# Performance work log

Measured on AMD Instinct MI355X. Metric: run time of the kernel, lower is better.

## Reference

```python
import jax, jax.numpy as jnp
import numpy as np

T, B, D, H = 4096, 4, 1024, 16


def setup_inputs() -> dict:
    key = jax.random.key(0)
    k0, k1, k2 = jax.random.split(key, 3)
    x = jax.random.normal(k0, (T, B, D), jnp.float32)
    Wqkv = jax.random.normal(k1, (3 * D, D), jnp.float32) * 0.02
    bqkv = jnp.zeros((3 * D,), jnp.float32)
    Wout = jax.random.normal(k2, (D, D), jnp.float32) * 0.02
    bout = jnp.zeros((D,), jnp.float32)
    return {"x": x, "Wqkv": Wqkv, "bqkv": bqkv, "Wout": Wout, "bout": bout, "nhead": H}


def reference(x, Wqkv, bqkv, Wout, bout, nhead):
    # x: (T, B, D) seq-first, query is key is value
    T_, B_, D_ = x.shape
    hd = D_ // nhead
    qkv = x @ Wqkv.T + bqkv                      # (T, B, 3D)
    q, k, v = jnp.split(qkv, 3, axis=-1)         # each (T, B, D)

    def heads(t):                                 # -> (B, H, T, hd)
        return t.reshape(T_, B_, nhead, hd).transpose(1, 2, 0, 3)

    q, k, v = heads(q), heads(k), heads(v)

    # Pearson correlation over the sequence axis: X, Y are (B, H, hd, T)
    X = jnp.swapaxes(q, -2, -1)
    Y = jnp.swapaxes(k, -2, -1)
    Xc = X - X.mean(-1, keepdims=True)
    Yc = Y - Y.mean(-1, keepdims=True)
    c = jnp.einsum('bhdt,bhet->bhde', Xc, Yc)    # (B, H, hd, hd)
    sx = (Xc ** 2).sum(-1)                       # (B, H, hd)
    sy = (Yc ** 2).sum(-1)                       # (B, H, hd)
    std = jnp.sqrt(sx[..., :, None] * sy[..., None, :])
    corr = jnp.clip(c / std, -1.0, 1.0)          # (B, H, hd, hd)

    attn = jnp.einsum('bhtd,bhde->bhte', v, corr)  # v @ corr: (B, H, T, hd)
    out = attn.transpose(2, 0, 1, 3).reshape(T_, B_, D_)  # (T, B, D)
    return out @ Wout.T + bout
```

## Files before the change

### kernel.cpp

```cpp
#include <hip/hip_runtime.h>
#include <hip/hip_bf16.h>

#define TDIM 4096
#define BDIM 4
#define DDIM 1024
#define HDIM 16
#define HD   64
#define MDIM (TDIM * BDIM)

typedef __attribute__((ext_vector_type(8))) short short8v;
typedef __attribute__((ext_vector_type(4))) float f32x4;

__device__ __forceinline__ ushort f2bfu(float f) {
  union { __hip_bfloat16 h; ushort u; } c;
  c.h = __float2bfloat16(f);
  return c.u;
}
__device__ __forceinline__ float bfu2f(ushort u) {
  union { ushort u; __hip_bfloat16 h; } c;
  c.u = u;
  return __bfloat162float(c.h);
}

#define GLOAD16(gp, lp) __builtin_amdgcn_global_load_lds( \
    (const __attribute__((address_space(1))) void*)(gp),  \
    (__attribute__((address_space(3))) void*)(lp), 16, 0, 0)

#define SWZ(row) (((row) >> 1) & 3)

__global__ __launch_bounds__(256)
void split_f32(const float* __restrict__ in, ushort* __restrict__ hi,
               ushort* __restrict__ lo, int n4)
{
  int i = blockIdx.x * blockDim.x + threadIdx.x;
  const int stride = gridDim.x * blockDim.x;
  for (; i < n4; i += stride) {
    const float4 v = ((const float4*)in)[i];
    ushort4 h, l;
    h.x = f2bfu(v.x); l.x = f2bfu(v.x - bfu2f(h.x));
    h.y = f2bfu(v.y); l.y = f2bfu(v.y - bfu2f(h.y));
    h.z = f2bfu(v.z); l.z = f2bfu(v.z - bfu2f(h.z));
    h.w = f2bfu(v.w); l.w = f2bfu(v.w - bfu2f(h.w));
    ((ushort4*)hi)[i] = h;
    ((ushort4*)lo)[i] = l;
  }
}

__global__ __launch_bounds__(256, 2)
void gemm1_mfma(const float* __restrict__ X, const ushort* __restrict__ Wh,
                const ushort* __restrict__ Wl, const float* __restrict__ bias,
                float* __restrict__ QK, ushort* __restrict__ Vh,
                ushort* __restrict__ Vl)
{
  __shared__ ushort sAh[128][32], sAl[128][32], sBh[128][32], sBl[128][32];
  const int tid = threadIdx.x;
  const int lane = tid & 63, wid = tid >> 6;
  const int m0 = blockIdx.y * 128, n0 = blockIdx.x * 128;
  const int ar = tid >> 3, aq = tid & 7;
  const int wm = wid >> 1, wn = wid & 1;
  const int fr = lane & 15, kg = lane >> 4;

  f32x4 acc[4][4];
#pragma unroll
  for (int m = 0; m < 4; ++m)
#pragma unroll
    for (int n = 0; n < 4; ++n) acc[m][n] = (f32x4){0.f, 0.f, 0.f, 0.f};

  for (int k0 = 0; k0 < DDIM; k0 += 32) {
    float4 av[4];
#pragma unroll
    for (int i = 0; i < 4; ++i)
      av[i] = *(const float4*)&X[(size_t)(m0 + ar + i * 32) * DDIM + k0 + aq * 4];
#pragma unroll
    for (int j = 0; j < 4; ++j) {
      const int c = wid * 4 + j;
      const int r0 = (c & 7) * 16;
      const int row = r0 + (lane >> 2);
      const int s = lane & 3;
      const size_t goff = (size_t)(n0 + row) * DDIM + k0 + ((s ^ SWZ(row)) << 3);
      if (c < 8) GLOAD16(Wh + goff, &sBh[r0][0]);
      else       GLOAD16(Wl + goff, &sBl[r0][0]);
    }
#pragma unroll
    for (int i = 0; i < 4; ++i) {
      const int row = ar + i * 32;
      const int sl = (((aq >> 1) ^ SWZ(row)) << 3) + ((aq & 1) << 2);
      ushort4 hv, lv;
      hv.x = f2bfu(av[i].x); lv.x = f2bfu(av[i].x - bfu2f(hv.x));
      hv.y = f2bfu(av[i].y); lv.y = f2bfu(av[i].y - bfu2f(hv.y));
      hv.z = f2bfu(av[i].z); lv.z = f2bfu(av[i].z - bfu2f(hv.z));
      hv.w = f2bfu(av[i].w); lv.w = f2bfu(av[i].w - bfu2f(hv.w));
      *(ushort4*)&sAh[row][sl] = hv;
      *(ushort4*)&sAl[row][sl] = lv;
    }
    __syncthreads();

    short8v ah[4], al[4], bh[4], bl[4];
#pragma unroll
    for (int m = 0; m < 4; ++m) {
      const int row = wm * 64 + m * 16 + fr;
      const int so = (kg ^ SWZ(row)) << 3;
      ah[m] = *(const short8v*)&sAh[row][so];
      al[m] = *(const short8v*)&sAl[row][so];
    }
#pragma unroll
    for (int n = 0; n < 4; ++n) {
      const int col = wn * 64 + n * 16 + fr;
      const int so = (kg ^ SWZ(col)) << 3;
      bh[n] = *(const short8v*)&sBh[col][so];
      bl[n] = *(const short8v*)&sBl[col][so];
    }
#pragma unroll
    for (int m = 0; m < 4; ++m)
#pragma unroll
      for (int n = 0; n < 4; ++n) {
        acc[m][n] = __builtin_amdgcn_mfma_f32_16x16x32_bf16(ah[m], bh[n], acc[m][n], 0, 0, 0);
        acc[m][n] = __builtin_amdgcn_mfma_f32_16x16x32_bf16(ah[m], bl[n], acc[m][n], 0, 0, 0);
        acc[m][n] = __builtin_amdgcn_mfma_f32_16x16x32_bf16(al[m], bh[n], acc[m][n], 0, 0, 0);
      }
    __syncthreads();
  }

  const int isV = (n0 >= 2048);
#pragma unroll
  for (int m = 0; m < 4; ++m)
#pragma unroll
    for (int n = 0; n < 4; ++n) {
      const int col = n0 + wn * 64 + n * 16 + fr;
      const float bz = bias[col];
#pragma unroll
      for (int r = 0; r < 4; ++r) {
        const int row = m0 + wm * 64 + m * 16 + kg * 4 + r;
        const float v = acc[m][n][r] + bz;
        if (!isV) {
          QK[(size_t)row * 2048 + col] = v;
        } else {
          const size_t o = (size_t)row * 1024 + (col - 2048);
          const ushort h = f2bfu(v);
          Vh[o] = h;
          Vl[o] = f2bfu(v - bfu2f(h));
        }
      }
    }
}

__global__ __launch_bounds__(256, 2)
void gemm2_mfma(const ushort* __restrict__ Vh, const ushort* __restrict__ Vl,
                const ushort* __restrict__ Weh, const ushort* __restrict__ Wel,
                const float* __restrict__ bias, float* __restrict__ Out)
{
  __shared__ ushort sAh[128][32], sAl[128][32], sBh[128][32], sBl[128][32];
  const int tid = threadIdx.x;
  const int lane = tid & 63, wid = tid >> 6;
  const int m0 = blockIdx.y * 128, n0 = blockIdx.x * 128, bb = blockIdx.z;
  const int wm = wid >> 1, wn = wid & 1;
  const int fr = lane & 15, kg = lane >> 4;

  f32x4 acc[4][4];
#pragma unroll
  for (int m = 0; m < 4; ++m)
#pragma unroll
    for (int n = 0; n < 4; ++n) acc[m][n] = (f32x4){0.f, 0.f, 0.f, 0.f};

  const size_t wB = (size_t)bb * DDIM * DDIM;

  for (int k0 = 0; k0 < DDIM; k0 += 32) {
#pragma unroll
    for (int j = 0; j < 8; ++j) {
      const int r0 = j * 16;
      const int row = r0 + (lane >> 2);
      const int s = lane & 3;
      const int ks = k0 + ((s ^ SWZ(row)) << 3);
      if (wid == 0)
        GLOAD16(Vh + (size_t)((m0 + row) * 4 + bb) * 1024 + ks, &sAh[r0][0]);
      else if (wid == 1)
        GLOAD16(Vl + (size_t)((m0 + row) * 4 + bb) * 1024 + ks, &sAl[r0][0]);
      else if (wid == 2)
        GLOAD16(Weh + wB + (size_t)(n0 + row) * 1024 + ks, &sBh[r0][0]);
      else
        GLOAD16(Wel + wB + (size_t)(n0 + row) * 1024 + ks, &sBl[r0][0]);
    }
    __syncthreads();

    short8v ah[4], al[4], bh[4], bl[4];
#pragma unroll
    for (int m = 0; m < 4; ++m) {
      const int row = wm * 64 + m * 16 + fr;
      const int so = (kg ^ SWZ(row)) << 3;
      ah[m] = *(const short8v*)&sAh[row][so];
      al[m] = *(const short8v*)&sAl[row][so];
    }
#pragma unroll
    for (int n = 0; n < 4; ++n) {
      const int col = wn * 64 + n * 16 + fr;
      const int so = (kg ^ SWZ(col)) << 3;
      bh[n] = *(const short8v*)&sBh[col][so];
      bl[n] = *(const short8v*)&sBl[col][so];
    }
#pragma unroll
    for (int m = 0; m < 4; ++m)
#pragma unroll
      for (int n = 0; n < 4; ++n) {
        acc[m][n] = __builtin_amdgcn_mfma_f32_16x16x32_bf16(ah[m], bh[n], acc[m][n], 0, 0, 0);
        acc[m][n] = __builtin_amdgcn_mfma_f32_16x16x32_bf16(ah[m], bl[n], acc[m][n], 0, 0, 0);
        acc[m][n] = __builtin_amdgcn_mfma_f32_16x16x32_bf16(al[m], bh[n], acc[m][n], 0, 0, 0);
      }
    __syncthreads();
  }

  float* Ob = Out + (size_t)bb * 1024;
#pragma unroll
  for (int m = 0; m < 4; ++m)
#pragma unroll
    for (int n = 0; n < 4; ++n) {
      const int col = n0 + wn * 64 + n * 16 + fr;
      const float bz = bias[col];
#pragma unroll
      for (int r = 0; r < 4; ++r) {
        const int row = m0 + wm * 64 + m * 16 + kg * 4 + r;
        Ob[(size_t)row * 4096 + col] = acc[m][n][r] + bz;
      }
    }
}

__global__ __launch_bounds__(256)
void corr_partial(const float* __restrict__ QK, float* __restrict__ P)
{
  __shared__ float qs[4][16][64];
  __shared__ float ks[4][16][64];
  __shared__ float ssum[4][4][64];
  const int bh  = blockIdx.x;
  const int seg = blockIdx.y;
  const int b = bh >> 4;
  const int h = bh & 15;
  const int tid = threadIdx.x;
  const int wid = tid >> 6, lane = tid & 63;
  const float* qb = QK + (size_t)b * 2048 + h * HD;
  const float* kb = qb + 1024;
  const int ty = lane >> 3;
  const int tx = lane & 7;
  const int rr = lane >> 4;
  const int cq = lane & 15;

  float acc[8][8];
#pragma unroll
  for (int i = 0; i < 8; ++i)
#pragma unroll
    for (int j = 0; j < 8; ++j) acc[i][j] = 0.f;
  float sQ[4]  = {0,0,0,0}, sK[4]  = {0,0,0,0};
  float sQ2[4] = {0,0,0,0}, sK2[4] = {0,0,0,0};

  for (int c = 0; c < 4; ++c) {
    const int tbase = seg * 256 + wid * 64 + c * 16;
    float4 qv[4], kv[4];
#pragma unroll
    for (int i = 0; i < 4; ++i) {
      const size_t g = (size_t)(tbase + rr + i*4) * 8192 + cq * 4;
      qv[i] = *(const float4*)&qb[g];
      kv[i] = *(const float4*)&kb[g];
    }
#pragma unroll
    for (int i = 0; i < 4; ++i) {
      const int row = rr + i*4;
      *(float4*)&qs[wid][row][cq*4] = qv[i];
      *(float4*)&ks[wid][row][cq*4] = kv[i];
      sQ[0] += qv[i].x; sQ[1] += qv[i].y; sQ[2] += qv[i].z; sQ[3] += qv[i].w;
      sK[0] += kv[i].x; sK[1] += kv[i].y; sK[2] += kv[i].z; sK[3] += kv[i].w;
      sQ2[0] = fmaf(qv[i].x, qv[i].x, sQ2[0]); sQ2[1] = fmaf(qv[i].y, qv[i].y, sQ2[1]);
      sQ2[2] = fmaf(qv[i].z, qv[i].z, sQ2[2]); sQ2[3] = fmaf(qv[i].w, qv[i].w, sQ2[3]);
      sK2[0] = fmaf(kv[i].x, kv[i].x, sK2[0]); sK2[1] = fmaf(kv[i].y, kv[i].y, sK2[1]);
      sK2[2] = fmaf(kv[i].z, kv[i].z, sK2[2]); sK2[3] = fmaf(kv[i].w, kv[i].w, sK2[3]);
    }
#pragma unroll 8
    for (int t = 0; t < 16; ++t) {
      const float4 qa  = *(const float4*)&qs[wid][t][ty*8];
      const float4 qb4 = *(const float4*)&qs[wid][t][ty*8+4];
      const float4 ka  = *(const float4*)&ks[wid][t][tx*8];
      const float4 kb4 = *(const float4*)&ks[wid][t][tx*8+4];
      const float av[8] = {qa.x, qa.y, qa.z, qa.w, qb4.x, qb4.y, qb4.z, qb4.w};
      const float bv[8] = {ka.x, ka.y, ka.z, ka.w, kb4.x, kb4.y, kb4.z, kb4.w};
#pragma unroll
      for (int i = 0; i < 8; ++i)
#pragma unroll
        for (int j = 0; j < 8; ++j)
          acc[i][j] = fmaf(av[i], bv[j], acc[i][j]);
    }
  }

#pragma unroll
  for (int j = 0; j < 4; ++j) {
    sQ[j]  += __shfl_xor(sQ[j], 16, 64);  sQ[j]  += __shfl_xor(sQ[j], 32, 64);
    sK[j]  += __shfl_xor(sK[j], 16, 64);  sK[j]  += __shfl_xor(sK[j], 32, 64);
    sQ2[j] += __shfl_xor(sQ2[j], 16, 64); sQ2[j] += __shfl_xor(sQ2[j], 32, 64);
    sK2[j] += __shfl_xor(sK2[j], 16, 64); sK2[j] += __shfl_xor(sK2[j], 32, 64);
  }
  if (lane < 16) {
    float4 q4; q4.x = sQ[0];  q4.y = sQ[1];  q4.z = sQ[2];  q4.w = sQ[3];
    float4 k4; k4.x = sK[0];  k4.y = sK[1];  k4.z = sK[2];  k4.w = sK[3];
    float4 q2; q2.x = sQ2[0]; q2.y = sQ2[1]; q2.z = sQ2[2]; q2.w = sQ2[3];
    float4 k2; k2.x = sK2[0]; k2.y = sK2[1]; k2.z = sK2[2]; k2.w = sK2[3];
    *(float4*)&ssum[wid][0][lane*4] = q4;
    *(float4*)&ssum[wid][1][lane*4] = k4;
    *(float4*)&ssum[wid][2][lane*4] = q2;
    *(float4*)&ssum[wid][3][lane*4] = k2;
  }

  float* cbuf = &qs[0][0][0];
  __syncthreads();
#pragma unroll
  for (int w = 0; w < 4; ++w) {
    if (wid == w) {
#pragma unroll
      for (int i = 0; i < 8; ++i) {
        float* p0 = &cbuf[(ty*8 + i) * 64 + tx*8];
        if (w == 0) {
          float4 o0, o1;
          o0.x = acc[i][0]; o0.y = acc[i][1]; o0.z = acc[i][2]; o0.w = acc[i][3];
          o1.x = acc[i][4]; o1.y = acc[i][5]; o1.z = acc[i][6]; o1.w = acc[i][7];
          *(float4*)p0 = o0; *(float4*)(p0 + 4) = o1;
        } else {
          float4 o0 = *(const float4*)p0, o1 = *(const float4*)(p0 + 4);
          o0.x += acc[i][0]; o0.y += acc[i][1]; o0.z += acc[i][2]; o0.w += acc[i][3];
          o1.x += acc[i][4]; o1.y += acc[i][5]; o1.z += acc[i][6]; o1.w += acc[i][7];
          *(float4*)p0 = o0; *(float4*)(p0 + 4) = o1;
        }
      }
    }
    __syncthreads();
  }

  float* Pb = P + (size_t)(bh * 16 + seg) * 4352;
#pragma unroll
  for (int i = 0; i < 4; ++i)
    ((float4*)Pb)[tid + 256*i] = ((const float4*)cbuf)[tid + 256*i];
  {
    const int comp = tid >> 6, d = tid & 63;
    Pb[4096 + tid] = ssum[0][comp][d] + ssum[1][comp][d] +
                     ssum[2][comp][d] + ssum[3][comp][d];
  }
}

__global__ __launch_bounds__(256)
void corr_finalize(const float* __restrict__ P, float* __restrict__ corr)
{
  __shared__ float fin[4][64];
  const int bh = blockIdx.x;
  const int tid = threadIdx.x;
  const float* Pb = P + (size_t)bh * 16 * 4352;

  float s = 0.f;
  for (int seg = 0; seg < 16; ++seg) s += Pb[(size_t)seg*4352 + 4096 + tid];
  fin[tid >> 6][tid & 63] = s;

  float cacc[16];
#pragma unroll
  for (int i = 0; i < 16; ++i) cacc[i] = 0.f;
  for (int seg = 0; seg < 16; ++seg) {
#pragma unroll
    for (int i = 0; i < 16; ++i)
      cacc[i] += Pb[(size_t)seg*4352 + tid + i*256];
  }
  __syncthreads();

  const float invT = 1.0f / (float)TDIM;
#pragma unroll
  for (int i = 0; i < 16; ++i) {
    const int f = tid + i*256;
    const int d = f >> 6, e = f & 63;
    const float sq = fin[0][d], sk = fin[1][e];
    const float sq2 = fin[2][d], sk2 = fin[3][e];
    const float cc = cacc[i] - sq * sk * invT;
    const float sx = sq2 - sq * sq * invT;
    const float sy = sk2 - sk * sk * invT;
    float v = cc / sqrtf(sx * sy);
    v = fminf(1.f, fmaxf(-1.f, v));
    corr[(size_t)bh * 4096 + f] = v;
  }
}

__global__ __launch_bounds__(256)
void weff_kernel(const float* __restrict__ corr, const float* __restrict__ Wout,
                 float* __restrict__ Weff)
{
  __shared__ float cs[64][64];
  __shared__ float ws[128][64];
  const int bh = blockIdx.x;
  const int b = bh >> 4, h = bh & 15;
  const int n0 = blockIdx.y * 128;
  const int tid = threadIdx.x;

  const float* cb = corr + (size_t)bh * 4096;
  float4* csv = (float4*)&cs[0][0];
#pragma unroll
  for (int i = 0; i < 4; ++i)
    csv[tid + 256*i] = ((const float4*)cb)[tid + 256*i];

  const int wr = tid >> 1, wh = (tid & 1) * 32;
  const float* wrow = Wout + (size_t)(n0 + wr) * DDIM + h * HD + wh;
#pragma unroll
  for (int i = 0; i < 8; ++i)
    *(float4*)&ws[wr][wh + i*4] = *(const float4*)&wrow[i*4];
  __syncthreads();

  const int ni = (tid >> 3) * 4;
  const int di = (tid & 7) * 8;
  float acc[4][8];
#pragma unroll
  for (int i = 0; i < 4; ++i)
#pragma unroll
    for (int j = 0; j < 8; ++j) acc[i][j] = 0.f;

  for (int e = 0; e < 64; ++e) {
    float wv[4], cv[8];
#pragma unroll
    for (int i = 0; i < 4; ++i) wv[i] = ws[ni + i][e];
#pragma unroll
    for (int j = 0; j < 8; ++j) cv[j] = cs[di + j][e];
#pragma unroll
    for (int i = 0; i < 4; ++i)
#pragma unroll
      for (int j = 0; j < 8; ++j)
        acc[i][j] = fmaf(wv[i], cv[j], acc[i][j]);
  }

  float* Wb = Weff + (size_t)b * DDIM * DDIM + h * HD;
#pragma unroll
  for (int i = 0; i < 4; ++i) {
    float4 o0, o1;
    o0.x = acc[i][0]; o0.y = acc[i][1]; o0.z = acc[i][2]; o0.w = acc[i][3];
    o1.x = acc[i][4]; o1.y = acc[i][5]; o1.z = acc[i][6]; o1.w = acc[i][7];
    *(float4*)&Wb[(size_t)(n0 + ni + i) * DDIM + di]     = o0;
    *(float4*)&Wb[(size_t)(n0 + ni + i) * DDIM + di + 4] = o1;
  }
}

extern "C" void kernel_launch(void* const* d_in, const int* in_sizes, int n_in,
                              void* d_out, int out_size, void* d_ws, size_t ws_size,
                              hipStream_t stream)
{
  (void)in_sizes; (void)n_in; (void)out_size; (void)ws_size;
  const float* x    = (const float*)d_in[0];
  const float* Wqkv = (const float*)d_in[1];
  const float* bqkv = (const float*)d_in[2];
  const float* Wout = (const float*)d_in[3];
  const float* bout = (const float*)d_in[4];
  float* out = (float*)d_out;

  char* w = (char*)d_ws;
  float*  QK    = (float*)w;   w += (size_t)134217728;
  ushort* Vh    = (ushort*)w;  w += (size_t)33554432;
  ushort* Vl    = (ushort*)w;  w += (size_t)33554432;
  float*  corrB = (float*)w;   w += (size_t)1048576;
  char* R1 = w;                w += (size_t)17825792;
  char* R2 = w;
  ushort* Wqh   = (ushort*)R1;
  ushort* Wql   = Wqh + (size_t)3145728;
  float*  P     = (float*)R1;
  float*  WeffF = (float*)R1;
  ushort* Weh   = (ushort*)R2;
  ushort* Wel   = Weh + (size_t)4194304;

  split_f32<<<dim3(1024), 256, 0, stream>>>(Wqkv, Wqh, Wql, 786432);
  gemm1_mfma<<<dim3(24, 128), 256, 0, stream>>>(x, Wqh, Wql, bqkv, QK, Vh, Vl);
  corr_partial<<<dim3(64, 16), 256, 0, stream>>>(QK, P);
  corr_finalize<<<dim3(64), 256, 0, stream>>>(P, corrB);
  weff_kernel<<<dim3(64, 8), 256, 0, stream>>>(corrB, Wout, WeffF);
  split_f32<<<dim3(1024), 256, 0, stream>>>(WeffF, Weh, Wel, 1048576);
  gemm2_mfma<<<dim3(8, 32, 4), 256, 0, stream>>>(Vh, Vl, Weh, Wel, bout, out);
}
```

Before: 659.2 us.

## Write Q/K head-major from GEMM1 and split corr_finalize across four blocks per head

The QKV GEMM epilogue now scatters Q and K into per-(batch,head) contiguous (T,64) buffers instead of a row-major (T*B, 2048) array. The correlation-partial kernel therefore reads contiguous 256-byte rows rather than rows strided 32 KB apart, which should improve its global-load locality. The finalize kernel is launched with four blocks per head, each handling a quarter of the 64x64 output, to add parallelism. In exchange, the GEMM epilogue stores become more scattered, with consecutive rows landing in different head buffers.

```diff
diff --git a/kernel.cpp b/kernel.cpp
--- a/kernel.cpp
+++ b/kernel.cpp
@@ -49,8 +49,8 @@
 __global__ __launch_bounds__(256, 2)
 void gemm1_mfma(const float* __restrict__ X, const ushort* __restrict__ Wh,
                 const ushort* __restrict__ Wl, const float* __restrict__ bias,
-                float* __restrict__ QK, ushort* __restrict__ Vh,
-                ushort* __restrict__ Vl)
+                float* __restrict__ Qc, float* __restrict__ Kc,
+                ushort* __restrict__ Vh, ushort* __restrict__ Vl)
 {
   __shared__ ushort sAh[128][32], sAl[128][32], sBh[128][32], sBl[128][32];
   const int tid = threadIdx.x;
@@ -121,24 +121,28 @@
     __syncthreads();
   }
 
-  const int isV = (n0 >= 2048);
+  const int region = n0 >> 10;
 #pragma unroll
   for (int m = 0; m < 4; ++m)
 #pragma unroll
     for (int n = 0; n < 4; ++n) {
       const int col = n0 + wn * 64 + n * 16 + fr;
       const float bz = bias[col];
+      const int cc = col & 1023;
+      const int hh = cc >> 6, dd = cc & 63;
 #pragma unroll
       for (int r = 0; r < 4; ++r) {
         const int row = m0 + wm * 64 + m * 16 + kg * 4 + r;
         const float v = acc[m][n][r] + bz;
-        if (!isV) {
-          QK[(size_t)row * 2048 + col] = v;
-        } else {
-          const size_t o = (size_t)row * 1024 + (col - 2048);
-          const ushort h = f2bfu(v);
-          Vh[o] = h;
-          Vl[o] = f2bfu(v - bfu2f(h));
+        const int t = row >> 2, b = row & 3;
+        const size_t ho = (((size_t)(b * 16 + hh)) * 4096 + t) * 64 + dd;
+        if (region == 0)      Qc[ho] = v;
+        else if (region == 1) Kc[ho] = v;
+        else {
+          const size_t o = (size_t)row * 1024 + cc;
+          const ushort h2 = f2bfu(v);
+          Vh[o] = h2;
+          Vl[o] = f2bfu(v - bfu2f(h2));
         }
       }
     }
@@ -224,19 +228,18 @@
 }
 
 __global__ __launch_bounds__(256)
-void corr_partial(const float* __restrict__ QK, float* __restrict__ P)
+void corr_partial(const float* __restrict__ Qc, const float* __restrict__ Kc,
+                  float* __restrict__ P)
 {
   __shared__ float qs[4][16][64];
   __shared__ float ks[4][16][64];
   __shared__ float ssum[4][4][64];
   const int bh  = blockIdx.x;
   const int seg = blockIdx.y;
-  const int b = bh >> 4;
-  const int h = bh & 15;
   const int tid = threadIdx.x;
   const int wid = tid >> 6, lane = tid & 63;
-  const float* qb = QK + (size_t)b * 2048 + h * HD;
-  const float* kb = qb + 1024;
+  const float* qb = Qc + (size_t)bh * 262144;
+  const float* kb = Kc + (size_t)bh * 262144;
   const int ty = lane >> 3;
   const int tx = lane & 7;
   const int rr = lane >> 4;
@@ -255,7 +258,7 @@
     float4 qv[4], kv[4];
 #pragma unroll
     for (int i = 0; i < 4; ++i) {
-      const size_t g = (size_t)(tbase + rr + i*4) * 8192 + cq * 4;
+      const size_t g = (size_t)(tbase + rr + i*4) * 64 + cq * 4;
       qv[i] = *(const float4*)&qb[g];
       kv[i] = *(const float4*)&kb[g];
     }
@@ -344,7 +347,7 @@
 void corr_finalize(const float* __restrict__ P, float* __restrict__ corr)
 {
   __shared__ float fin[4][64];
-  const int bh = blockIdx.x;
+  const int bh = blockIdx.x, qtr = blockIdx.y;
   const int tid = threadIdx.x;
   const float* Pb = P + (size_t)bh * 16 * 4352;
 
@@ -352,20 +355,18 @@
   for (int seg = 0; seg < 16; ++seg) s += Pb[(size_t)seg*4352 + 4096 + tid];
   fin[tid >> 6][tid & 63] = s;
 
-  float cacc[16];
-#pragma unroll
-  for (int i = 0; i < 16; ++i) cacc[i] = 0.f;
+  float cacc[4] = {0.f, 0.f, 0.f, 0.f};
   for (int seg = 0; seg < 16; ++seg) {
 #pragma unroll
-    for (int i = 0; i < 16; ++i)
-      cacc[i] += Pb[(size_t)seg*4352 + tid + i*256];
+    for (int i = 0; i < 4; ++i)
+      cacc[i] += Pb[(size_t)seg*4352 + qtr*1024 + tid + i*256];
   }
   __syncthreads();
 
   const float invT = 1.0f / (float)TDIM;
 #pragma unroll
-  for (int i = 0; i < 16; ++i) {
-    const int f = tid + i*256;
+  for (int i = 0; i < 4; ++i) {
+    const int f = qtr*1024 + tid + i*256;
     const int d = f >> 6, e = f & 63;
     const float sq = fin[0][d], sk = fin[1][e];
     const float sq2 = fin[2][d], sk2 = fin[3][e];
@@ -447,7 +448,8 @@
   float* out = (float*)d_out;
 
   char* w = (char*)d_ws;
-  float*  QK    = (float*)w;   w += (size_t)134217728;
+  float*  Qc    = (float*)w;   w += (size_t)67108864;
+  float*  Kc    = (float*)w;   w += (size_t)67108864;
   ushort* Vh    = (ushort*)w;  w += (size_t)33554432;
   ushort* Vl    = (ushort*)w;  w += (size_t)33554432;
   float*  corrB = (float*)w;   w += (size_t)1048576;
@@ -461,9 +463,9 @@
   ushort* Wel   = Weh + (size_t)4194304;
 
   split_f32<<<dim3(1024), 256, 0, stream>>>(Wqkv, Wqh, Wql, 786432);
-  gemm1_mfma<<<dim3(24, 128), 256, 0, stream>>>(x, Wqh, Wql, bqkv, QK, Vh, Vl);
-  corr_partial<<<dim3(64, 16), 256, 0, stream>>>(QK, P);
-  corr_finalize<<<dim3(64), 256, 0, stream>>>(P, corrB);
+  gemm1_mfma<<<dim3(24, 128), 256, 0, stream>>>(x, Wqh, Wql, bqkv, Qc, Kc, Vh, Vl);
+  corr_partial<<<dim3(64, 16), 256, 0, stream>>>(Qc, Kc, P);
+  corr_finalize<<<dim3(64, 4), 256, 0, stream>>>(P, corrB);
   weff_kernel<<<dim3(64, 8), 256, 0, stream>>>(corrB, Wout, WeffF);
   split_f32<<<dim3(1024), 256, 0, stream>>>(WeffF, Weh, Wel, 1048576);
   gemm2_mfma<<<dim3(8, 32, 4), 256, 0, stream>>>(Vh, Vl, Weh, Wel, bout, out);
```

Result: no change. 657.7 us (-0.2%).
